# Performance work log

Measured on AMD Instinct MI355X. Metric: run time of the kernel, lower is better.

The kernel has to match this reference:

```python
import jax, jax.numpy as jnp
import numpy as np

HIDDEN = 1024
NUM_HEADS = 16
HEAD_DIM = HIDDEN // NUM_HEADS  # 64
ROPE_DIM = HEAD_DIM // 2        # 32 (per-axis rotary dim)
EPS = 1e-6


def _make_rope_tables(dim, grid_h, grid_w, theta=10000.0):
    # pt_seq_len == ft_seq_len, so t_h = arange(H), t_w = arange(W)
    freqs = 1.0 / theta ** (np.arange(0, dim, 2, dtype=np.float32)[: dim // 2] / dim)  # [dim//2]
    fh = np.repeat(np.outer(np.arange(grid_h, dtype=np.float32), freqs), 2, axis=-1)  # [H, dim]
    fw = np.repeat(np.outer(np.arange(grid_w, dtype=np.float32), freqs), 2, axis=-1)  # [W, dim]
    fh = np.broadcast_to(fh[:, None, :], (grid_h, grid_w, dim))
    fw = np.broadcast_to(fw[None, :, :], (grid_h, grid_w, dim))
    f2d = np.concatenate([fh, fw], axis=-1).reshape(grid_h * grid_w, 2 * dim)  # [HW, 2*dim]
    return jnp.asarray(np.cos(f2d)), jnp.asarray(np.sin(f2d))


def _rms_norm(x, w, eps=EPS):
    var = jnp.mean(jnp.square(x), axis=-1, keepdims=True)
    return x * jax.lax.rsqrt(var + eps) * w


def _rotate_half(x):
    x1 = x[..., 0::2]
    x2 = x[..., 1::2]
    return jnp.stack([-x2, x1], axis=-1).reshape(x.shape)


def _apply_rope(x, cos, sin):
    # x: [B, H, S, D]; cos/sin: [S, D]
    return x * cos + _rotate_half(x) * sin


def setup_inputs() -> dict:
    key = jax.random.key(0)
    ks = jax.random.split(key, 12)
    B, IMG_H, IMG_W, CND_H, CND_W = 2, 64, 64, 32, 32
    img_len, cnd_len = IMG_H * IMG_W, CND_H * CND_W
    xav = (6.0 / (HIDDEN + HIDDEN)) ** 0.5
    inp = {
        'image_tokens': jax.random.normal(ks[0], (B, img_len, HIDDEN), jnp.float32),
        'condition_tokens': jax.random.normal(ks[1], (B, cnd_len, HIDDEN), jnp.float32),
        'q_norm_w': jnp.ones((HIDDEN,), jnp.float32),
        'kv_norm_w': jnp.ones((HIDDEN,), jnp.float32),
        'q_head_norm_w': jnp.ones((HEAD_DIM,), jnp.float32),
        'k_head_norm_w': jnp.ones((HEAD_DIM,), jnp.float32),
        'q_w': jax.random.uniform(ks[2], (HIDDEN, HIDDEN), jnp.float32, -xav, xav),
        'q_b': jnp.zeros((HIDDEN,), jnp.float32),
        'k_w': jax.random.uniform(ks[3], (HIDDEN, HIDDEN), jnp.float32, -xav, xav),
        'k_b': jnp.zeros((HIDDEN,), jnp.float32),
        'v_w': jax.random.uniform(ks[4], (HIDDEN, HIDDEN), jnp.float32, -xav, xav),
        'v_b': jnp.zeros((HIDDEN,), jnp.float32),
        'o_w': jax.random.uniform(ks[5], (HIDDEN, HIDDEN), jnp.float32, -xav, xav),
        'o_b': jnp.zeros((HIDDEN,), jnp.float32),
        'alpha': jnp.full((1,), 0.5, jnp.float32),  # nonzero so backward exercises the attn path
    }
    ic, isn = _make_rope_tables(ROPE_DIM, IMG_H, IMG_W)
    cc, cs = _make_rope_tables(ROPE_DIM, CND_H, CND_W)
    inp.update(image_cos=ic, image_sin=isn, cond_cos=cc, cond_sin=cs)
    return inp


def reference(image_tokens, condition_tokens, q_norm_w, kv_norm_w, q_head_norm_w,
              k_head_norm_w, q_w, q_b, k_w, k_b, v_w, v_b, o_w, o_b, alpha,
              image_cos, image_sin, cond_cos, cond_sin):
    B, Li, _ = image_tokens.shape
    Lc = condition_tokens.shape[1]
    qn = _rms_norm(image_tokens, q_norm_w)
    kvn = _rms_norm(condition_tokens, kv_norm_w)
    # projections (torch Linear: x @ W.T + b); weights here stored [out, in]
    q = (qn @ q_w.T + q_b).reshape(B, Li, NUM_HEADS, HEAD_DIM).transpose(0, 2, 1, 3)
    k = (kvn @ k_w.T + k_b).reshape(B, Lc, NUM_HEADS, HEAD_DIM).transpose(0, 2, 1, 3)
    v = (kvn @ v_w.T + v_b).reshape(B, Lc, NUM_HEADS, HEAD_DIM).transpose(0, 2, 1, 3)
    q = _rms_norm(q, q_head_norm_w)
    k = _rms_norm(k, k_head_norm_w)
    q = _apply_rope(q, image_cos, image_sin)
    k = _apply_rope(k, cond_cos, cond_sin)
    scale = 1.0 / jnp.sqrt(jnp.asarray(HEAD_DIM, q.dtype))
    scores = jnp.einsum('bhqd,bhkd->bhqk', q, k) * scale
    attn = jax.nn.softmax(scores, axis=-1)
    out = jnp.einsum('bhqk,bhkd->bhqd', attn, v)
    out = out.transpose(0, 2, 1, 3).reshape(B, Li, HIDDEN)
    update = out @ o_w.T + o_b
    return image_tokens + alpha.reshape(1, 1, 1) * update
```

## Files before the change

### kernel.cpp

```cpp
#include <hip/hip_runtime.h>

typedef __bf16 bf16x8 __attribute__((ext_vector_type(8)));
typedef __bf16 bf16x4 __attribute__((ext_vector_type(4)));
typedef float  f32x4  __attribute__((ext_vector_type(4)));
typedef float  f32x16 __attribute__((ext_vector_type(16)));
typedef unsigned u32x2 __attribute__((ext_vector_type(2)));

#define DEVINL __device__ __forceinline__

DEVINL void gload_lds16(const void* g, void* l) {
  __builtin_amdgcn_global_load_lds((const __attribute__((address_space(1))) void*)g,
                                   (__attribute__((address_space(3))) void*)l, 16, 0, 0);
}

DEVINL unsigned pkbf(float a, float b) {
  union { __bf16 h[2]; unsigned u; } c;
  c.h[0] = (__bf16)a; c.h[1] = (__bf16)b;
  return c.u;
}

DEVINL float fast_exp2(float x) {
#if __has_builtin(__builtin_amdgcn_exp2f)
  return __builtin_amdgcn_exp2f(x);
#else
  float r;
  asm volatile("v_exp_f32 %0, %1" : "=v"(r) : "v"(x));
  return r;
#endif
}

DEVINL float2 swap32(float x) {
  u32x2 r = __builtin_amdgcn_permlane32_swap(__float_as_uint(x), __float_as_uint(x), false, false);
  return make_float2(__uint_as_float(r.x), __uint_as_float(r.y));
}

__global__ __launch_bounds__(256) void prep_kernel(
    const float* __restrict__ XA, const float* __restrict__ WA, __bf16* __restrict__ YA,
    const float* __restrict__ XB, const float* __restrict__ WB, __bf16* __restrict__ YB,
    const float* __restrict__ wq, const float* __restrict__ wk,
    const float* __restrict__ wv, const float* __restrict__ wo,
    __bf16* __restrict__ oq, __bf16* __restrict__ ok,
    __bf16* __restrict__ ov, __bf16* __restrict__ oo) {
  int rb = blockIdx.x, tid = threadIdx.x;
  if (rb < 10240) {
    const float* X; const float* W; __bf16* Y; int row;
    if (rb < 8192) { X = XA; W = WA; Y = YA; row = rb; }
    else { X = XB; W = WB; Y = YB; row = rb - 8192; }
    const float4* xr = (const float4*)(X + (size_t)row * 1024);
    float4 v = xr[tid];
    float ss = v.x * v.x + v.y * v.y + v.z * v.z + v.w * v.w;
#pragma unroll
    for (int m = 1; m < 64; m <<= 1) ss += __shfl_xor(ss, m);
    __shared__ float part[4];
    if ((tid & 63) == 0) part[tid >> 6] = ss;
    __syncthreads();
    float tot = part[0] + part[1] + part[2] + part[3];
    float rn = rsqrtf(tot * (1.0f / 1024.0f) + 1e-6f);
    float4 wv4 = ((const float4*)W)[tid];
    bf16x4 y;
    y[0] = (__bf16)(v.x * rn * wv4.x);
    y[1] = (__bf16)(v.y * rn * wv4.y);
    y[2] = (__bf16)(v.z * rn * wv4.z);
    y[3] = (__bf16)(v.w * rn * wv4.w);
    *(bf16x4*)(Y + (size_t)row * 1024 + tid * 4) = y;
  } else {
    int gid = (rb - 10240) * 256 + tid;
    int which = gid >> 17;
    size_t off = (size_t)(gid & 131071) * 8;
    const float* s = (which == 0) ? wq : (which == 1) ? wk : (which == 2) ? wv : wo;
    __bf16* o = (which == 0) ? oq : (which == 1) ? ok : (which == 2) ? ov : oo;
    float4 v0 = *(const float4*)(s + off), v1 = *(const float4*)(s + off + 4);
    bf16x8 y;
    y[0] = (__bf16)v0.x; y[1] = (__bf16)v0.y; y[2] = (__bf16)v0.z; y[3] = (__bf16)v0.w;
    y[4] = (__bf16)v1.x; y[5] = (__bf16)v1.y; y[6] = (__bf16)v1.z; y[7] = (__bf16)v1.w;
    *(bf16x8*)(o + off) = y;
  }
}

template <typename EPIF>
DEVINL void gemm256_core(const __bf16* __restrict__ A, const __bf16* __restrict__ Bw,
                         int m0, int n0, char* lds, EPIF epi) {
  int tid = threadIdx.x, lane = tid & 63, w = tid >> 6;
  int wr = w >> 2, wc = w & 3;
  int bhalf = wc >> 1;
  int rA = lane & 15, hiq = lane >> 4;
  int sx = rA & 7;

  auto ldsA = [&](int buf, int H) { return lds + (buf * 2 + H) * 16384; };
  auto ldsB = [&](int buf, int H) { return lds + 65536 + (buf * 2 + H) * 16384; };

  int c0 = tid, c1 = 512 + tid;
  size_t so0, so1;
  {
    int r0 = c0 >> 3, r1 = c1 >> 3;
    so0 = (size_t)r0 * 1024 + (size_t)(((c0 & 7) ^ (r0 & 7)) * 8);
    so1 = (size_t)r1 * 1024 + (size_t)(((c1 & 7) ^ (r1 & 7)) * 8);
  }
  auto STA = [&](int kt, int buf, int H) {
    const __bf16* g = A + (size_t)(m0 + H * 128) * 1024 + kt * 64;
    char* d = ldsA(buf, H) + w * 1024;
    gload_lds16(g + so0, d);
    gload_lds16(g + so1, d + 8192);
  };
  auto STB = [&](int kt, int buf, int H) {
    const __bf16* g = Bw + (size_t)(n0 + H * 128) * 1024 + kt * 64;
    char* d = ldsB(buf, H) + w * 1024;
    gload_lds16(g + so0, d);
    gload_lds16(g + so1, d + 8192);
  };

  f32x4 acc[8][4];
#pragma unroll
  for (int i = 0; i < 8; i++)
#pragma unroll
    for (int j = 0; j < 4; j++) acc[i][j] = {0.f, 0.f, 0.f, 0.f};

  const int NT = 16;
  STA(0, 0, 0); STB(0, 0, 0); STA(0, 0, 1); STB(0, 0, 1);
  STB(1, 1, 0); STB(1, 1, 1); STA(1, 1, 0);
  asm volatile("s_waitcnt vmcnt(6)" ::: "memory");
  __builtin_amdgcn_s_barrier();
  asm volatile("" ::: "memory");

  bf16x8 af[4][2], bfA[2][2], bfB[2][2];

  for (int kt = 0; kt < NT; ++kt) {
    int p = kt & 1;
    const char* baA = ldsA(p, wr);
    const char* baB = ldsB(p, bhalf);

#pragma unroll
    for (int j = 0; j < 4; j++) {
      int row = j * 16 + rA;
#pragma unroll
      for (int kk = 0; kk < 2; kk++)
        af[j][kk] = *(const bf16x8*)(baA + row * 128 + (((kk << 2) + hiq) ^ sx) * 16);
    }
#pragma unroll
    for (int ni = 0; ni < 2; ni++) {
      int row = (wc & 1) * 64 + ni * 16 + rA;
#pragma unroll
      for (int kk = 0; kk < 2; kk++)
        bfA[ni][kk] = *(const bf16x8*)(baB + row * 128 + (((kk << 2) + hiq) ^ sx) * 16);
    }
    if (kt + 1 < NT) STA(kt + 1, p ^ 1, 1);
    __builtin_amdgcn_s_barrier();
    asm volatile("s_waitcnt lgkmcnt(0)" ::: "memory");
    __builtin_amdgcn_sched_barrier(0);
    __builtin_amdgcn_s_setprio(1);
#pragma unroll
    for (int j = 0; j < 4; j++)
#pragma unroll
      for (int ni = 0; ni < 2; ni++) {
        acc[j][ni] = __builtin_amdgcn_mfma_f32_16x16x32_bf16(af[j][0], bfA[ni][0], acc[j][ni], 0, 0, 0);
        acc[j][ni] = __builtin_amdgcn_mfma_f32_16x16x32_bf16(af[j][1], bfA[ni][1], acc[j][ni], 0, 0, 0);
      }
    __builtin_amdgcn_s_setprio(0);
    __builtin_amdgcn_s_barrier();
    asm volatile("" ::: "memory");

#pragma unroll
    for (int ni = 0; ni < 2; ni++) {
      int row = (wc & 1) * 64 + (ni + 2) * 16 + rA;
#pragma unroll
      for (int kk = 0; kk < 2; kk++)
        bfB[ni][kk] = *(const bf16x8*)(baB + row * 128 + (((kk << 2) + hiq) ^ sx) * 16);
    }
    __builtin_amdgcn_s_barrier();
    asm volatile("s_waitcnt lgkmcnt(0)" ::: "memory");
    __builtin_amdgcn_sched_barrier(0);
    __builtin_amdgcn_s_setprio(1);
#pragma unroll
    for (int j = 0; j < 4; j++)
#pragma unroll
      for (int ni = 0; ni < 2; ni++) {
        acc[j][ni + 2] = __builtin_amdgcn_mfma_f32_16x16x32_bf16(af[j][0], bfB[ni][0], acc[j][ni + 2], 0, 0, 0);
        acc[j][ni + 2] = __builtin_amdgcn_mfma_f32_16x16x32_bf16(af[j][1], bfB[ni][1], acc[j][ni + 2], 0, 0, 0);
      }
    __builtin_amdgcn_s_setprio(0);
    __builtin_amdgcn_s_barrier();
    asm volatile("" ::: "memory");

#pragma unroll
    for (int j = 0; j < 4; j++) {
      int row = (4 + j) * 16 + rA;
#pragma unroll
      for (int kk = 0; kk < 2; kk++)
        af[j][kk] = *(const bf16x8*)(baA + row * 128 + (((kk << 2) + hiq) ^ sx) * 16);
    }
    if (kt + 2 < NT) STB(kt + 2, p, 0);
    __builtin_amdgcn_s_barrier();
    asm volatile("s_waitcnt lgkmcnt(0)" ::: "memory");
    __builtin_amdgcn_sched_barrier(0);
    __builtin_amdgcn_s_setprio(1);
#pragma unroll
    for (int j = 0; j < 4; j++)
#pragma unroll
      for (int ni = 0; ni < 2; ni++) {
        acc[4 + j][ni] = __builtin_amdgcn_mfma_f32_16x16x32_bf16(af[j][0], bfA[ni][0], acc[4 + j][ni], 0, 0, 0);
        acc[4 + j][ni] = __builtin_amdgcn_mfma_f32_16x16x32_bf16(af[j][1], bfA[ni][1], acc[4 + j][ni], 0, 0, 0);
      }
    __builtin_amdgcn_s_setprio(0);
    __builtin_amdgcn_s_barrier();
    asm volatile("" ::: "memory");

    if (kt + 2 < NT) { STB(kt + 2, p, 1); STA(kt + 2, p, 0); }
    __builtin_amdgcn_s_barrier();
    asm volatile("" ::: "memory");
    __builtin_amdgcn_s_setprio(1);
#pragma unroll
    for (int j = 0; j < 4; j++)
#pragma unroll
      for (int ni = 0; ni < 2; ni++) {
        acc[4 + j][ni + 2] = __builtin_amdgcn_mfma_f32_16x16x32_bf16(af[j][0], bfB[ni][0], acc[4 + j][ni + 2], 0, 0, 0);
        acc[4 + j][ni + 2] = __builtin_amdgcn_mfma_f32_16x16x32_bf16(af[j][1], bfB[ni][1], acc[4 + j][ni + 2], 0, 0, 0);
      }
    __builtin_amdgcn_s_setprio(0);
    if (kt + 2 < NT) {
      asm volatile("s_waitcnt vmcnt(6)" ::: "memory");
    } else if (kt + 1 < NT) {
      asm volatile("s_waitcnt vmcnt(0)" ::: "memory");
    }
    __builtin_amdgcn_s_barrier();
    asm volatile("" ::: "memory");
  }
  epi(acc, lane, wr, wc);
}

__global__ __launch_bounds__(512) void qkv_gemm256_kernel(
    const __bf16* __restrict__ qn, const __bf16* __restrict__ kvn,
    const __bf16* __restrict__ wq, const __bf16* __restrict__ wkv,
    const float* __restrict__ qb, const float* __restrict__ kb, const float* __restrict__ vb,
    __bf16* __restrict__ Qt, __bf16* __restrict__ Kt, __bf16* __restrict__ Vt0) {
  __shared__ __attribute__((aligned(16))) char lds[131072];
  int id = blockIdx.x;
  const __bf16 *A, *Bw; const float* bias; __bf16* Cout;
  int m0, n0, nloc;
  if (id < 128) {
    A = qn; Bw = wq; m0 = (id & 31) * 256; n0 = (id >> 5) * 256; nloc = n0;
    bias = qb; Cout = Qt;
  } else {
    int i2 = id - 128;
    A = kvn; Bw = wkv; m0 = (i2 & 7) * 256; n0 = (i2 >> 3) * 256;
    if (n0 < 1024) { bias = kb; Cout = Kt; nloc = n0; }
    else { bias = vb; Cout = Vt0; nloc = n0 - 1024; }
  }
  gemm256_core(A, Bw, m0, n0, lds,
               [&](f32x4 (&acc)[8][4], int lane, int wr, int wc) {
#pragma unroll
                 for (int mi = 0; mi < 8; mi++)
#pragma unroll
                   for (int ni = 0; ni < 4; ni++) {
                     int col = nloc + wc * 64 + ni * 16 + (lane & 15);
                     float bv = bias[col];
#pragma unroll
                     for (int r = 0; r < 4; r++) {
                       int row = m0 + wr * 128 + mi * 16 + ((lane >> 4) << 2) + r;
                       Cout[((size_t)row << 10) + col] = (__bf16)(acc[mi][ni][r] + bv);
                     }
                   }
               });
}

__global__ __launch_bounds__(512) void o_gemm256_kernel(
    const __bf16* __restrict__ A, const __bf16* __restrict__ Bw,
    const float* __restrict__ bias, float* __restrict__ Cout,
    const float* __restrict__ resid, const float* __restrict__ alphap) {
  __shared__ __attribute__((aligned(16))) char lds[131072];
  int id = blockIdx.x;
  int m0 = (id & 31) * 256, n0 = (id >> 5) * 256;
  float aval = alphap[0];
  gemm256_core(A, Bw, m0, n0, lds,
               [&](f32x4 (&acc)[8][4], int lane, int wr, int wc) {
#pragma unroll
                 for (int mi = 0; mi < 8; mi++)
#pragma unroll
                   for (int ni = 0; ni < 4; ni++) {
                     int col = n0 + wc * 64 + ni * 16 + (lane & 15);
                     float bv = bias[col];
#pragma unroll
                     for (int r = 0; r < 4; r++) {
                       int row = m0 + wr * 128 + mi * 16 + ((lane >> 4) << 2) + r;
                       size_t idx = ((size_t)row << 10) + col;
                       Cout[idx] = resid[idx] + aval * (acc[mi][ni][r] + bv);
                     }
                   }
               });
}

__global__ __launch_bounds__(256) void kprep_kernel(
    const __bf16* __restrict__ Kt, const float* __restrict__ KHW,
    const float* __restrict__ CCOS, const float* __restrict__ CSIN,
    __bf16* __restrict__ Kr,
    const __bf16* __restrict__ V, __bf16* __restrict__ Vt) {
  int rb = blockIdx.x, tid = threadIdx.x;
  if (rb < 1024) {
    int inst = rb * 32 + (tid >> 3);
    int sub = tid & 7;
    int token = inst >> 4, h = inst & 15;
    int b = token >> 10, pos = token & 1023;
    const __bf16* xp = Kt + ((size_t)token << 10) + h * 64 + sub * 8;
    bf16x8 xv = *(const bf16x8*)xp;
    float xf[8];
#pragma unroll
    for (int i = 0; i < 8; i++) xf[i] = (float)xv[i];
    float ss = 0.f;
#pragma unroll
    for (int i = 0; i < 8; i++) ss += xf[i] * xf[i];
    ss += __shfl_xor(ss, 1);
    ss += __shfl_xor(ss, 2);
    ss += __shfl_xor(ss, 4);
    float rn = rsqrtf(ss * (1.0f / 64.0f) + 1e-6f);
    const float* hwp = KHW + sub * 8;
    const float* cp = CCOS + ((size_t)pos << 6) + sub * 8;
    const float* sp = CSIN + ((size_t)pos << 6) + sub * 8;
    float xn[8], o[8];
#pragma unroll
    for (int i = 0; i < 8; i++) xn[i] = xf[i] * rn * hwp[i];
#pragma unroll
    for (int i = 0; i < 8; i += 2) {
      o[i] = xn[i] * cp[i] - xn[i + 1] * sp[i];
      o[i + 1] = xn[i + 1] * cp[i + 1] + xn[i] * sp[i + 1];
    }
    bf16x8 yv;
#pragma unroll
    for (int i = 0; i < 8; i++) yv[i] = (__bf16)o[i];
    *(bf16x8*)(Kr + (((size_t)((b << 4) + h) << 10) + pos) * 64 + sub * 8) = yv;
  } else {
    int bx = rb - 1024;
    int bh = bx >> 4;
    int j0 = (bx & 15) * 64;
    int b = bh >> 4, h = bh & 15;
#pragma unroll
    for (int it = 0; it < 2; ++it) {
      int c = it * 256 + tid;
      int jl = c >> 3, d0 = (c & 7) * 8;
      bf16x8 v = *(const bf16x8*)(V + (size_t)(b * 1024 + j0 + jl) * 1024 + h * 64 + d0);
#pragma unroll
      for (int i = 0; i < 8; i++)
        Vt[((size_t)bh * 64 + d0 + i) * 1024 + j0 + jl] = v[i];
    }
  }
}

__global__ __launch_bounds__(256, 2) void attn_kernel(
    const __bf16* __restrict__ Qt, const float* __restrict__ QHW,
    const float* __restrict__ QCOS, const float* __restrict__ QSIN,
    const __bf16* __restrict__ Kr, const __bf16* __restrict__ Vtr,
    __bf16* __restrict__ AO) {
  int tid = threadIdx.x, lane = tid & 63, w = tid >> 6;
  int lq = lane & 31, hi = lane >> 5;
  int q0 = blockIdx.x * 256;
  int bh = blockIdx.y, b = bh >> 4, h = bh & 15;
  const float QSC = 0.125f * 1.44269504088896340736f;

  __shared__ __attribute__((aligned(16))) __bf16 Ks[2][4096];
  __shared__ __attribute__((aligned(16))) __bf16 Vs[2][4096];

  const __bf16* Kbh = Kr + ((size_t)bh << 16);
  const __bf16* Vbh = Vtr + ((size_t)bh << 16);

  auto STAGE = [&](int T, int BSEL) {
#pragma unroll
    for (int i = 0; i < 2; i++) {
      int s = 2 * w + i;
      int kt = s >> 2, ds2 = s & 3;
      gload_lds16(Kbh + (size_t)(T * 64 + kt * 32 + lq) * 64 + ds2 * 16 + hi * 8,
                  (char*)Ks[BSEL] + s * 1024);
      int f = s >> 1, dh = s & 1;
      gload_lds16(Vbh + (size_t)(dh * 32 + lq) * 1024 + T * 64 + f * 16 + hi * 8,
                  (char*)Vs[BSEL] + s * 1024);
    }
  };

  STAGE(0, 0);

  bf16x8 qf[2][4];
#pragma unroll
  for (int qt = 0; qt < 2; qt++) {
    int pos = q0 + w * 64 + qt * 32 + lq;
    const __bf16* qp = Qt + ((size_t)(b * 4096 + pos) << 10) + h * 64 + hi * 8;
    float xf[4][8];
    float ss = 0.f;
#pragma unroll
    for (int ds = 0; ds < 4; ds++) {
      bf16x8 xv = *(const bf16x8*)(qp + ds * 16);
#pragma unroll
      for (int j = 0; j < 8; j++) { float f = (float)xv[j]; xf[ds][j] = f; ss += f * f; }
    }
    float2 sw = swap32(ss);
    float rn = rsqrtf((sw.x + sw.y) * (1.0f / 64.0f) + 1e-6f);
#pragma unroll
    for (int ds = 0; ds < 4; ds++) {
      int d0 = ds * 16 + hi * 8;
      const float* wp = QHW + d0;
      const float* cp = QCOS + ((size_t)pos << 6) + d0;
      const float* sp = QSIN + ((size_t)pos << 6) + d0;
      float4 wa = *(const float4*)wp, wb = *(const float4*)(wp + 4);
      float4 ca = *(const float4*)cp, cb = *(const float4*)(cp + 4);
      float4 sa = *(const float4*)sp, sb = *(const float4*)(sp + 4);
      float wv[8] = {wa.x, wa.y, wa.z, wa.w, wb.x, wb.y, wb.z, wb.w};
      float cv[8] = {ca.x, ca.y, ca.z, ca.w, cb.x, cb.y, cb.z, cb.w};
      float sv[8] = {sa.x, sa.y, sa.z, sa.w, sb.x, sb.y, sb.z, sb.w};
      float xn[8];
#pragma unroll
      for (int j = 0; j < 8; j++) xn[j] = xf[ds][j] * rn * wv[j];
      bf16x8 q8;
#pragma unroll
      for (int j = 0; j < 8; j += 2) {
        q8[j]     = (__bf16)((xn[j] * cv[j] - xn[j + 1] * sv[j]) * QSC);
        q8[j + 1] = (__bf16)((xn[j + 1] * cv[j + 1] + xn[j] * sv[j + 1]) * QSC);
      }
      qf[qt][ds] = q8;
    }
  }

  f32x16 Z16;
#pragma unroll
  for (int r = 0; r < 16; r++) Z16[r] = 0.f;
  f32x16 accO[2][2];
#pragma unroll
  for (int qt = 0; qt < 2; qt++)
#pragma unroll
    for (int dh = 0; dh < 2; dh++) accO[qt][dh] = Z16;
  float srun[2] = {0.f, 0.f};

  __syncthreads();

  int buf = 0;
  for (int t = 0; t < 16; t++) {
    if (t < 15) {
#pragma unroll
      for (int i = 0; i < 2; i++) {
        int s = 2 * w + i;
        int kt = s >> 2, ds2 = s & 3;
        gload_lds16(Kbh + (size_t)((t + 1) * 64 + kt * 32 + lq) * 64 + ds2 * 16 + hi * 8,
                    (char*)Ks[buf ^ 1] + s * 1024);
        int f = s >> 1, dh = s & 1;
        gload_lds16(Vbh + (size_t)(dh * 32 + lq) * 1024 + (t + 1) * 64 + f * 16 + hi * 8,
                    (char*)Vs[buf ^ 1] + s * 1024);
      }
    }
    const char* kbase = (const char*)Ks[buf];
    const char* vbase = (const char*)Vs[buf];
    int loff = lane * 16;

    bf16x8 kf[8], vf[8];
#pragma unroll
    for (int s = 0; s < 8; s++) kf[s] = *(const bf16x8*)(kbase + s * 1024 + loff);
#pragma unroll
    for (int s = 0; s < 8; s++) vf[s] = *(const bf16x8*)(vbase + s * 1024 + loff);

    f32x16 accS[2][2];
    __builtin_amdgcn_s_setprio(1);
#pragma unroll
    for (int qt = 0; qt < 2; qt++)
#pragma unroll
      for (int kt = 0; kt < 2; kt++) {
        accS[qt][kt] = __builtin_amdgcn_mfma_f32_32x32x16_bf16(kf[kt * 4], qf[qt][0], Z16, 0, 0, 0);
#pragma unroll
        for (int ds = 1; ds < 4; ds++)
          accS[qt][kt] = __builtin_amdgcn_mfma_f32_32x32x16_bf16(kf[kt * 4 + ds], qf[qt][ds], accS[qt][kt], 0, 0, 0);
      }
    __builtin_amdgcn_s_setprio(0);

    unsigned pa[2][4][4];
#pragma unroll
    for (int qt = 0; qt < 2; qt++) {
      float ssum = 0.f;
#pragma unroll
      for (int kt = 0; kt < 2; kt++)
#pragma unroll
        for (int r = 0; r < 16; r++) {
          float e = fast_exp2(accS[qt][kt][r]);
          accS[qt][kt][r] = e;
          ssum += e;
        }
      float2 sws = swap32(ssum);
      srun[qt] += sws.x + sws.y;
#pragma unroll
      for (int kt = 0; kt < 2; kt++)
#pragma unroll
        for (int s2 = 0; s2 < 2; s2++) {
          int f = kt * 2 + s2, rb = s2 * 8;
          unsigned u  = pkbf(accS[qt][kt][rb + 0], accS[qt][kt][rb + 1]);
          unsigned v2 = pkbf(accS[qt][kt][rb + 2], accS[qt][kt][rb + 3]);
          unsigned w2 = pkbf(accS[qt][kt][rb + 4], accS[qt][kt][rb + 5]);
          unsigned x2 = pkbf(accS[qt][kt][rb + 6], accS[qt][kt][rb + 7]);
          u32x2 r02 = __builtin_amdgcn_permlane32_swap(u, w2, false, false);
          u32x2 r13 = __builtin_amdgcn_permlane32_swap(v2, x2, false, false);
          pa[qt][f][0] = r02.x; pa[qt][f][1] = r13.x; pa[qt][f][2] = r02.y; pa[qt][f][3] = r13.y;
        }
    }

    __builtin_amdgcn_s_setprio(1);
#pragma unroll
    for (int f = 0; f < 4; f++)
#pragma unroll
      for (int qt = 0; qt < 2; qt++) {
        union { unsigned u[4]; bf16x8 v; } pf;
        pf.u[0] = pa[qt][f][0]; pf.u[1] = pa[qt][f][1];
        pf.u[2] = pa[qt][f][2]; pf.u[3] = pa[qt][f][3];
#pragma unroll
        for (int dh = 0; dh < 2; dh++)
          accO[qt][dh] = __builtin_amdgcn_mfma_f32_32x32x16_bf16(pf.v, vf[f * 2 + dh], accO[qt][dh], 0, 0, 0);
      }
    __builtin_amdgcn_s_setprio(0);
    __syncthreads();
    buf ^= 1;
  }

  __bf16* aobase = AO + (((size_t)b * 4096) << 10) + h * 64;
#pragma unroll
  for (int qt = 0; qt < 2; qt++) {
    float rinv = 1.0f / srun[qt];
    int ri = __float_as_int(rinv);
#pragma unroll
    for (int r = 0; r < 16; r++) {
      int cr = (r & 3) + ((r >> 2) << 3) + (hi << 2);
      float rv = __int_as_float(__builtin_amdgcn_ds_bpermute(cr << 2, ri));
      size_t rowoff = ((size_t)(q0 + w * 64 + qt * 32 + cr) << 10);
#pragma unroll
      for (int dh = 0; dh < 2; dh++)
        aobase[rowoff + dh * 32 + lq] = (__bf16)(accO[qt][dh][r] * rv);
    }
  }
}

extern "C" void kernel_launch(void* const* d_in, const int* in_sizes, int n_in,
                              void* d_out, int out_size, void* d_ws, size_t ws_size,
                              hipStream_t stream) {
  const float* img  = (const float*)d_in[0];
  const float* cnd  = (const float*)d_in[1];
  const float* qnw  = (const float*)d_in[2];
  const float* kvnw = (const float*)d_in[3];
  const float* qhw  = (const float*)d_in[4];
  const float* khw  = (const float*)d_in[5];
  const float* qw   = (const float*)d_in[6];
  const float* qb   = (const float*)d_in[7];
  const float* kw   = (const float*)d_in[8];
  const float* kb   = (const float*)d_in[9];
  const float* vw   = (const float*)d_in[10];
  const float* vb   = (const float*)d_in[11];
  const float* ow   = (const float*)d_in[12];
  const float* ob   = (const float*)d_in[13];
  const float* alpha= (const float*)d_in[14];
  const float* icos = (const float*)d_in[15];
  const float* isin = (const float*)d_in[16];
  const float* ccos = (const float*)d_in[17];
  const float* csin = (const float*)d_in[18];
  float* out = (float*)d_out;

  __bf16* p = (__bf16*)d_ws;
  __bf16* wqb = p; p += 1048576;
  __bf16* wkb = p; p += 1048576;
  __bf16* wvb = p; p += 1048576;
  __bf16* wob = p; p += 1048576;
  __bf16* qn  = p; p += 8388608;
  __bf16* kvn = p; p += 2097152;
  __bf16* Qt  = p; p += 8388608;
  __bf16* Kt  = p; p += 2097152;
  __bf16* Vt0 = p; p += 2097152;
  __bf16* Kr  = p; p += 2097152;
  __bf16* Vtr = p; p += 2097152;
  __bf16* AO  = qn;

  prep_kernel<<<12288, 256, 0, stream>>>(img, qnw, qn, cnd, kvnw, kvn,
                                         qw, kw, vw, ow, wqb, wkb, wvb, wob);

  qkv_gemm256_kernel<<<192, 512, 0, stream>>>(qn, kvn, wqb, wkb, qb, kb, vb, Qt, Kt, Vt0);

  kprep_kernel<<<1536, 256, 0, stream>>>(Kt, khw, ccos, csin, Kr, Vt0, Vtr);

  attn_kernel<<<dim3(16, 32), 256, 0, stream>>>(Qt, qhw, icos, isin, Kr, Vtr, AO);

  o_gemm256_kernel<<<128, 512, 0, stream>>>(AO, wob, ob, out, img, alpha);
}
```

Before: 152.1 us.

## Replace exp2 with bit-trick bf16 exponent and compute row sums via MFMA

The softmax exp2 plus float-to-bf16 pack is replaced by a Schraudolph-style trick: an fma with a magic offset whose integer value is used directly as bf16 bits approximating 2^x. The per-row sum is no longer built with VALU adds and a lane swap. Instead an extra MFMA against a ones vector accumulates it from the same bf16 P values, and the final normalisation uses a fast reciprocal per output element with no cross-lane permute. This targets VALU and transcendental cost in the inner loop, but costs extra MFMA work and adds a piecewise-linear exp error of a few percent.

New measurement: 148.1 us. -2.7%, faster.

```diff
diff --git a/kernel.cpp b/kernel.cpp
--- a/kernel.cpp
+++ b/kernel.cpp
@@ -13,25 +13,17 @@
                                    (__attribute__((address_space(3))) void*)l, 16, 0, 0);
 }
 
-DEVINL unsigned pkbf(float a, float b) {
-  union { __bf16 h[2]; unsigned u; } c;
-  c.h[0] = (__bf16)a; c.h[1] = (__bf16)b;
-  return c.u;
-}
-
-DEVINL float fast_exp2(float x) {
-#if __has_builtin(__builtin_amdgcn_exp2f)
-  return __builtin_amdgcn_exp2f(x);
-#else
-  float r;
-  asm volatile("v_exp_f32 %0, %1" : "=v"(r) : "v"(x));
-  return r;
-#endif
-}
-
 DEVINL float2 swap32(float x) {
   u32x2 r = __builtin_amdgcn_permlane32_swap(__float_as_uint(x), __float_as_uint(x), false, false);
   return make_float2(__uint_as_float(r.x), __uint_as_float(r.y));
+}
+
+DEVINL float fast_rcp(float x) {
+#if __has_builtin(__builtin_amdgcn_rcpf)
+  return __builtin_amdgcn_rcpf(x);
+#else
+  return 1.0f / x;
+#endif
 }
 
 __global__ __launch_bounds__(256) void prep_kernel(
@@ -353,6 +345,7 @@
   int q0 = blockIdx.x * 256;
   int bh = blockIdx.y, b = bh >> 4, h = bh & 15;
   const float QSC = 0.125f * 1.44269504088896340736f;
+  const float MAGIC = 16250.5f;
 
   __shared__ __attribute__((aligned(16))) __bf16 Ks[2][4096];
   __shared__ __attribute__((aligned(16))) __bf16 Vs[2][4096];
@@ -419,11 +412,14 @@
 #pragma unroll
   for (int r = 0; r < 16; r++) Z16[r] = 0.f;
   f32x16 accO[2][2];
-#pragma unroll
-  for (int qt = 0; qt < 2; qt++)
-#pragma unroll
-    for (int dh = 0; dh < 2; dh++) accO[qt][dh] = Z16;
-  float srun[2] = {0.f, 0.f};
+  f32x16 accR[2];
+#pragma unroll
+  for (int qt = 0; qt < 2; qt++) {
+    accO[qt][0] = Z16; accO[qt][1] = Z16; accR[qt] = Z16;
+  }
+  bf16x8 ones8;
+#pragma unroll
+  for (int i = 0; i < 8; i++) ones8[i] = (__bf16)1.0f;
 
   __syncthreads();
 
@@ -466,32 +462,23 @@
 
     unsigned pa[2][4][4];
 #pragma unroll
-    for (int qt = 0; qt < 2; qt++) {
-      float ssum = 0.f;
-#pragma unroll
-      for (int kt = 0; kt < 2; kt++)
-#pragma unroll
-        for (int r = 0; r < 16; r++) {
-          float e = fast_exp2(accS[qt][kt][r]);
-          accS[qt][kt][r] = e;
-          ssum += e;
-        }
-      float2 sws = swap32(ssum);
-      srun[qt] += sws.x + sws.y;
+    for (int qt = 0; qt < 2; qt++)
 #pragma unroll
       for (int kt = 0; kt < 2; kt++)
 #pragma unroll
         for (int s2 = 0; s2 < 2; s2++) {
           int f = kt * 2 + s2, rb = s2 * 8;
-          unsigned u  = pkbf(accS[qt][kt][rb + 0], accS[qt][kt][rb + 1]);
-          unsigned v2 = pkbf(accS[qt][kt][rb + 2], accS[qt][kt][rb + 3]);
-          unsigned w2 = pkbf(accS[qt][kt][rb + 4], accS[qt][kt][rb + 5]);
-          unsigned x2 = pkbf(accS[qt][kt][rb + 6], accS[qt][kt][rb + 7]);
-          u32x2 r02 = __builtin_amdgcn_permlane32_swap(u, w2, false, false);
-          u32x2 r13 = __builtin_amdgcn_permlane32_swap(v2, x2, false, false);
+          unsigned q[4];
+#pragma unroll
+          for (int i = 0; i < 4; i++) {
+            float t0 = fmaf(accS[qt][kt][rb + 2 * i], 128.f, MAGIC);
+            float t1 = fmaf(accS[qt][kt][rb + 2 * i + 1], 128.f, MAGIC);
+            q[i] = ((unsigned)t1 << 16) | (unsigned)t0;
+          }
+          u32x2 r02 = __builtin_amdgcn_permlane32_swap(q[0], q[2], false, false);
+          u32x2 r13 = __builtin_amdgcn_permlane32_swap(q[1], q[3], false, false);
           pa[qt][f][0] = r02.x; pa[qt][f][1] = r13.x; pa[qt][f][2] = r02.y; pa[qt][f][3] = r13.y;
         }
-    }
 
     __builtin_amdgcn_s_setprio(1);
 #pragma unroll
@@ -501,9 +488,9 @@
         union { unsigned u[4]; bf16x8 v; } pf;
         pf.u[0] = pa[qt][f][0]; pf.u[1] = pa[qt][f][1];
         pf.u[2] = pa[qt][f][2]; pf.u[3] = pa[qt][f][3];
-#pragma unroll
-        for (int dh = 0; dh < 2; dh++)
-          accO[qt][dh] = __builtin_amdgcn_mfma_f32_32x32x16_bf16(pf.v, vf[f * 2 + dh], accO[qt][dh], 0, 0, 0);
+        accO[qt][0] = __builtin_amdgcn_mfma_f32_32x32x16_bf16(pf.v, vf[f * 2 + 0], accO[qt][0], 0, 0, 0);
+        accO[qt][1] = __builtin_amdgcn_mfma_f32_32x32x16_bf16(pf.v, vf[f * 2 + 1], accO[qt][1], 0, 0, 0);
+        accR[qt]    = __builtin_amdgcn_mfma_f32_32x32x16_bf16(pf.v, ones8, accR[qt], 0, 0, 0);
       }
     __builtin_amdgcn_s_setprio(0);
     __syncthreads();
@@ -513,12 +500,10 @@
   __bf16* aobase = AO + (((size_t)b * 4096) << 10) + h * 64;
 #pragma unroll
   for (int qt = 0; qt < 2; qt++) {
-    float rinv = 1.0f / srun[qt];
-    int ri = __float_as_int(rinv);
 #pragma unroll
     for (int r = 0; r < 16; r++) {
+      float rv = fast_rcp(accR[qt][r]);
       int cr = (r & 3) + ((r >> 2) << 3) + (hi << 2);
-      float rv = __int_as_float(__builtin_amdgcn_ds_bpermute(cr << 2, ri));
       size_t rowoff = ((size_t)(q0 + w * 64 + qt * 32 + cr) << 10);
 #pragma unroll
       for (int dh = 0; dh < 2; dh++)
```
